# Performance work log

Hardware: AMD Instinct MI355X
Metric: run time of the kernel (lower is better)

The kernel has to match this reference:

```python
import jax, jax.numpy as jnp
import numpy as np

KS = 3          # ksize
PAD = 1         # (ksize-1)//2 * dilation, dilation=1

def setup_inputs() -> dict:
    key = jax.random.key(0)
    k1, k2, k3, k4 = jax.random.split(key, 4)
    B, NI, C, H, W = 4, 64, 64, 256, 256
    features = jax.random.normal(k1, (B, NI, H, W), jnp.float32)
    inpt = jax.random.normal(k2, (B, C, H, W), jnp.float32)
    # get_filter: Conv2d(ni, ksize**2, 3, padding=1 reflect, stride=1)
    w = jax.random.normal(k3, (KS * KS, NI, 3, 3), jnp.float32) * 0.05
    b = jax.random.normal(k4, (KS * KS,), jnp.float32) * 0.01
    return {"features": features, "inpt": inpt, "w": w, "b": b}

def reference(features, inpt, w, b):
    # 1) predict per-pixel filters: 3x3 conv with reflect padding
    fpad = jnp.pad(features, ((0, 0), (0, 0), (1, 1), (1, 1)), mode="reflect")
    ff = jax.lax.conv_general_dilated(
        fpad, w, window_strides=(1, 1), padding="VALID",
        dimension_numbers=("NCHW", "OIHW", "NCHW"),
    ) + b[None, :, None, None]                       # [B, 9, H, W]
    ff = jax.nn.softmax(ff, axis=1)                  # softmax over the 9 taps

    # 2) apply per-pixel filter to inpt (shared across channels)
    B, C, H, W = inpt.shape
    ipad = jnp.pad(inpt, ((0, 0), (0, 0), (PAD, PAD), (PAD, PAD)), mode="reflect")
    # unfold: taps in row-major (ki, kj) order, matching torch nn.Unfold
    patches = jnp.stack(
        [ipad[:, :, i:i + H, j:j + W] for i in range(KS) for j in range(KS)],
        axis=2,
    )                                                # [B, C, 9, H, W]
    # out[b,c,h,w] = sum_k patches[b,c,k,h,w] * ff[b,k,h,w]
    return jnp.einsum("bckhw,bkhw->bchw", patches, ff)
```

## Files before the change

### kernel.cpp

```cpp
#include <hip/hip_runtime.h>
#include <math.h>

#define BB 4
#define NI 64
#define CC 64
#define HH 256
#define WW 256

__device__ __forceinline__ int refl(int i, int n) {
    i = (i < 0) ? -i : i;
    return (i >= n) ? (2 * n - 2 - i) : i;
}

__global__ __launch_bounds__(256) void pff_fused(
    const float* __restrict__ features,
    const float* __restrict__ inpt,
    const float* __restrict__ wgt,
    const float* __restrict__ bias,
    float* __restrict__ out)
{
    const int tid = threadIdx.x;
    const int wx = blockIdx.x * 64 + (tid & 63);
    const int hy = blockIdx.y * 4 + (tid >> 6);
    const int b  = blockIdx.z;

    const int ih0 = refl(hy - 1, HH);
    const int ih1 = hy;
    const int ih2 = refl(hy + 1, HH);
    const int iw0 = refl(wx - 1, WW);
    const int iw1 = wx;
    const int iw2 = refl(wx + 1, WW);

    const int r0 = ih0 * WW, r1 = ih1 * WW, r2 = ih2 * WW;

    float acc[9];
    #pragma unroll
    for (int k = 0; k < 9; ++k) acc[k] = bias[k];

    const float* fb = features + (size_t)b * NI * HH * WW;
    for (int ni = 0; ni < NI; ++ni) {
        const float* fc = fb + (size_t)ni * HH * WW;
        float f[9];
        f[0] = fc[r0 + iw0]; f[1] = fc[r0 + iw1]; f[2] = fc[r0 + iw2];
        f[3] = fc[r1 + iw0]; f[4] = fc[r1 + iw1]; f[5] = fc[r1 + iw2];
        f[6] = fc[r2 + iw0]; f[7] = fc[r2 + iw1]; f[8] = fc[r2 + iw2];

        const float* wn = wgt + ni * 9;
        #pragma unroll
        for (int k = 0; k < 9; ++k) {
            const float* wk = wn + k * (NI * 9);
            #pragma unroll
            for (int t = 0; t < 9; ++t)
                acc[k] = fmaf(f[t], wk[t], acc[k]);
        }
    }

    float m = acc[0];
    #pragma unroll
    for (int k = 1; k < 9; ++k) m = fmaxf(m, acc[k]);
    float s = 0.f;
    #pragma unroll
    for (int k = 0; k < 9; ++k) { acc[k] = __expf(acc[k] - m); s += acc[k]; }
    const float inv = 1.f / s;
    #pragma unroll
    for (int k = 0; k < 9; ++k) acc[k] *= inv;

    const float* ib = inpt + (size_t)b * CC * HH * WW;
    float* ob = out + (size_t)b * CC * HH * WW;
    const size_t opix = (size_t)hy * WW + wx;
    for (int c = 0; c < CC; ++c) {
        const float* ic = ib + (size_t)c * HH * WW;
        float o = acc[0] * ic[r0 + iw0];
        o = fmaf(acc[1], ic[r0 + iw1], o);
        o = fmaf(acc[2], ic[r0 + iw2], o);
        o = fmaf(acc[3], ic[r1 + iw0], o);
        o = fmaf(acc[4], ic[r1 + iw1], o);
        o = fmaf(acc[5], ic[r1 + iw2], o);
        o = fmaf(acc[6], ic[r2 + iw0], o);
        o = fmaf(acc[7], ic[r2 + iw1], o);
        o = fmaf(acc[8], ic[r2 + iw2], o);
        ob[(size_t)c * HH * WW + opix] = o;
    }
}

extern "C" void kernel_launch(void* const* d_in, const int* in_sizes, int n_in,
                              void* d_out, int out_size, void* d_ws, size_t ws_size,
                              hipStream_t stream) {
    const float* features = (const float*)d_in[0];
    const float* inpt     = (const float*)d_in[1];
    const float* wgt      = (const float*)d_in[2];
    const float* bias     = (const float*)d_in[3];
    float* out            = (float*)d_out;

    dim3 grid(WW / 64, HH / 4, BB);
    dim3 block(256);
    pff_fused<<<grid, block, 0, stream>>>(features, inpt, wgt, bias, out);
}
```

Baseline: 83.08 us.

## Compute filter-prediction conv with bf16 MFMA from LDS-staged feature tiles

Replaces the scalar per-pixel 3x3x64 filter-prediction convolution with bf16 MFMA 16x16x32 instructions. Feature tiles with halo are staged into LDS as bf16, and the weights are pre-packed by a small prep kernel into an MFMA-ready table in workspace. Softmax is computed across lanes with shuffles, and the channel-application loop is split across waves with software prefetch of the next channel. This removes most of the FP32 FMA work and redundant global loads, at the cost of bf16 rounding in the logits and an extra kernel launch.

```diff
diff --git a/kernel.cpp b/kernel.cpp
--- a/kernel.cpp
+++ b/kernel.cpp
@@ -2,84 +2,170 @@
 #include <math.h>
 
 #define BB 4
-#define NI 64
+#define NIC 64
 #define CC 64
 #define HH 256
 #define WW 256
+#define HW (HH * WW)
+
+#define TCH 72
+
+typedef short sh8 __attribute__((ext_vector_type(8)));
+typedef float f32x4 __attribute__((ext_vector_type(4)));
 
 __device__ __forceinline__ int refl(int i, int n) {
     i = (i < 0) ? -i : i;
     return (i >= n) ? (2 * n - 2 - i) : i;
 }
+__device__ __forceinline__ unsigned short f2bf(float v) {
+    unsigned int x = __builtin_bit_cast(unsigned int, v);
+    return (unsigned short)((x + 0x7FFFu + ((x >> 16) & 1u)) >> 16);
+}
 
-__global__ __launch_bounds__(256) void pff_fused(
+__global__ void pff_prep(const float* __restrict__ wgt, uint4* __restrict__ wtab) {
+    int e = blockIdx.x * 256 + threadIdx.x;
+    if (e >= 18 * 64) return;
+    const int c = e >> 6, l = e & 63;
+    const int s = c >> 1, h = c & 1;
+    const int tap = l & 15, kg = l >> 4;
+    unsigned short bb16[8];
+    #pragma unroll
+    for (int j = 0; j < 8; ++j) {
+        const int ni = 32 * h + 8 * kg + j;
+        const float v = (tap <= 8) ? wgt[tap * 576 + ni * 9 + s] : 0.f;
+        bb16[j] = f2bf(v);
+    }
+    uint4 o;
+    o.x = bb16[0] | ((unsigned)bb16[1] << 16);
+    o.y = bb16[2] | ((unsigned)bb16[3] << 16);
+    o.z = bb16[4] | ((unsigned)bb16[5] << 16);
+    o.w = bb16[6] | ((unsigned)bb16[7] << 16);
+    wtab[e] = o;
+}
+
+__global__ __launch_bounds__(512) void pff_mfma(
     const float* __restrict__ features,
     const float* __restrict__ inpt,
-    const float* __restrict__ wgt,
     const float* __restrict__ bias,
+    const uint4* __restrict__ wtab,
     float* __restrict__ out)
 {
-    const int tid = threadIdx.x;
-    const int wx = blockIdx.x * 64 + (tid & 63);
-    const int hy = blockIdx.y * 4 + (tid >> 6);
-    const int b  = blockIdx.z;
+    __shared__ __align__(16) unsigned short T[4 * 66 * TCH];
+    __shared__ uint4 wtile[18 * 64];
+    __shared__ float ffl[9 * 128];
 
-    const int ih0 = refl(hy - 1, HH);
-    const int ih1 = hy;
-    const int ih2 = refl(hy + 1, HH);
-    const int iw0 = refl(wx - 1, WW);
-    const int iw1 = wx;
-    const int iw2 = refl(wx + 1, WW);
+    const int tid  = threadIdx.x;
+    const int wv   = __builtin_amdgcn_readfirstlane(tid >> 6);
+    const int lane = tid & 63;
+    const int W0 = blockIdx.x * 64;
+    const int H0 = blockIdx.y * 2;
+    const int bb = blockIdx.z;
 
-    const int r0 = ih0 * WW, r1 = ih1 * WW, r2 = ih2 * WW;
-
-    float acc[9];
+    const int kg  = lane >> 4;
+    const int pxl = lane & 15;
+    float bv4[4];
     #pragma unroll
-    for (int k = 0; k < 9; ++k) acc[k] = bias[k];
-
-    const float* fb = features + (size_t)b * NI * HH * WW;
-    for (int ni = 0; ni < NI; ++ni) {
-        const float* fc = fb + (size_t)ni * HH * WW;
-        float f[9];
-        f[0] = fc[r0 + iw0]; f[1] = fc[r0 + iw1]; f[2] = fc[r0 + iw2];
-        f[3] = fc[r1 + iw0]; f[4] = fc[r1 + iw1]; f[5] = fc[r1 + iw2];
-        f[6] = fc[r2 + iw0]; f[7] = fc[r2 + iw1]; f[8] = fc[r2 + iw2];
-
-        const float* wn = wgt + ni * 9;
-        #pragma unroll
-        for (int k = 0; k < 9; ++k) {
-            const float* wk = wn + k * (NI * 9);
-            #pragma unroll
-            for (int t = 0; t < 9; ++t)
-                acc[k] = fmaf(f[t], wk[t], acc[k]);
-        }
+    for (int j = 0; j < 4; ++j) {
+        const int tap = 4 * kg + j;
+        bv4[j] = bias[tap <= 8 ? tap : 8];
     }
 
-    float m = acc[0];
-    #pragma unroll
-    for (int k = 1; k < 9; ++k) m = fmaxf(m, acc[k]);
-    float s = 0.f;
-    #pragma unroll
-    for (int k = 0; k < 9; ++k) { acc[k] = __expf(acc[k] - m); s += acc[k]; }
-    const float inv = 1.f / s;
-    #pragma unroll
-    for (int k = 0; k < 9; ++k) acc[k] *= inv;
+    {
+        const int gc1 = refl(W0 - 1 + lane, WW);
+        const int gc2 = refl(W0 + 63 + lane, WW);
+        for (int it = wv; it < 256; it += 8) {
+            const int ch = it & 63, ri = it >> 6;
+            const int gr = refl(H0 - 1 + ri, HH);
+            const float* fp = features + ((bb * NIC + ch) * HH + gr) * WW;
+            const float v1 = fp[gc1];
+            T[(ri * 66 + lane) * TCH + ch] = f2bf(v1);
+            if (lane < 2) {
+                const float v2 = fp[gc2];
+                T[(ri * 66 + 64 + lane) * TCH + ch] = f2bf(v2);
+            }
+        }
+        for (int i = tid; i < 18 * 64; i += 512) wtile[i] = wtab[i];
+    }
+    __syncthreads();
 
-    const float* ib = inpt + (size_t)b * CC * HH * WW;
-    float* ob = out + (size_t)b * CC * HH * WW;
-    const size_t opix = (size_t)hy * WW + wx;
-    for (int c = 0; c < CC; ++c) {
-        const float* ic = ib + (size_t)c * HH * WW;
-        float o = acc[0] * ic[r0 + iw0];
-        o = fmaf(acc[1], ic[r0 + iw1], o);
-        o = fmaf(acc[2], ic[r0 + iw2], o);
-        o = fmaf(acc[3], ic[r1 + iw0], o);
-        o = fmaf(acc[4], ic[r1 + iw1], o);
-        o = fmaf(acc[5], ic[r1 + iw2], o);
-        o = fmaf(acc[6], ic[r2 + iw0], o);
-        o = fmaf(acc[7], ic[r2 + iw1], o);
-        o = fmaf(acc[8], ic[r2 + iw2], o);
-        ob[(size_t)c * HH * WW + opix] = o;
+    {
+        const int grow = wv & 1;
+        const int col0 = (wv >> 1) * 16;
+        f32x4 acc = {0.f, 0.f, 0.f, 0.f};
+        const int baseB = (grow * 66 + col0 + pxl) * TCH + 8 * kg;
+        #pragma unroll
+        for (int c = 0; c < 18; ++c) {
+            const int s = c >> 1, h = c & 1;
+            const int idx = baseB + ((s / 3) * 66 + (s % 3)) * TCH + 32 * h;
+            sh8 bv = *reinterpret_cast<const sh8*>(&T[idx]);
+            sh8 av = *reinterpret_cast<const sh8*>(&wtile[c * 64 + lane]);
+            acc = __builtin_amdgcn_mfma_f32_16x16x32_bf16(av, bv, acc, 0, 0, 0);
+        }
+        float lg[4];
+        bool val[4];
+        #pragma unroll
+        for (int j = 0; j < 4; ++j) {
+            const int tap = 4 * kg + j;
+            val[j] = (tap <= 8);
+            lg[j] = acc[j] + bv4[j];
+        }
+        float ml = -3e38f;
+        #pragma unroll
+        for (int j = 0; j < 4; ++j) ml = fmaxf(ml, val[j] ? lg[j] : -3e38f);
+        float m = fmaxf(ml, __shfl_xor(ml, 16));
+        m = fmaxf(m, __shfl_xor(m, 32));
+        float e[4], sl = 0.f;
+        #pragma unroll
+        for (int j = 0; j < 4; ++j) { e[j] = val[j] ? __expf(lg[j] - m) : 0.f; sl += e[j]; }
+        float s = sl + __shfl_xor(sl, 16);
+        s += __shfl_xor(s, 32);
+        const float inv = 1.f / s;
+        #pragma unroll
+        for (int j = 0; j < 4; ++j)
+            if (val[j]) ffl[(4 * kg + j) * 128 + grow * 64 + col0 + pxl] = e[j] * inv;
+    }
+    __syncthreads();
+
+    {
+        const int q = wv & 3;
+        const int r = wv >> 2;
+        const int wx = W0 + lane, py = H0 + r;
+        int go[9];
+        #pragma unroll
+        for (int i = 0; i < 3; ++i) {
+            const int rr = refl(py - 1 + i, HH) * WW;
+            #pragma unroll
+            for (int j = 0; j < 3; ++j) go[i * 3 + j] = rr + refl(wx - 1 + j, WW);
+        }
+        float ffv[9];
+        #pragma unroll
+        for (int k = 0; k < 9; ++k) ffv[k] = ffl[k * 128 + r * 64 + lane];
+
+        const float* ib = inpt + ((size_t)bb * CC + q * 16) * HW;
+        float* ob = out + ((size_t)bb * CC + q * 16) * HW + py * WW + wx;
+
+        float f[9], g[9];
+        #pragma unroll
+        for (int t = 0; t < 9; ++t) f[t] = ib[go[t]];
+        for (int chi = 0; chi < 16; ++chi) {
+            if (chi < 15) {
+                const float* i2 = ib + (size_t)(chi + 1) * HW;
+                #pragma unroll
+                for (int t = 0; t < 9; ++t) g[t] = i2[go[t]];
+            }
+            float o = ffv[0] * f[0];
+            o = fmaf(ffv[1], f[1], o);
+            o = fmaf(ffv[2], f[2], o);
+            o = fmaf(ffv[3], f[3], o);
+            o = fmaf(ffv[4], f[4], o);
+            o = fmaf(ffv[5], f[5], o);
+            o = fmaf(ffv[6], f[6], o);
+            o = fmaf(ffv[7], f[7], o);
+            o = fmaf(ffv[8], f[8], o);
+            ob[(size_t)chi * HW] = o;
+            #pragma unroll
+            for (int t = 0; t < 9; ++t) f[t] = g[t];
+        }
     }
 }
 
@@ -91,8 +177,11 @@
     const float* wgt      = (const float*)d_in[2];
     const float* bias     = (const float*)d_in[3];
     float* out            = (float*)d_out;
+    uint4* wtab           = (uint4*)d_ws;
 
-    dim3 grid(WW / 64, HH / 4, BB);
-    dim3 block(256);
-    pff_fused<<<grid, block, 0, stream>>>(features, inpt, wgt, bias, out);
+    pff_prep<<<dim3((18 * 64 + 255) / 256), dim3(256), 0, stream>>>(wgt, wtab);
+
+    dim3 grid(WW / 64, HH / 2, BB);
+    dim3 block(512);
+    pff_mfma<<<grid, block, 0, stream>>>(features, inpt, bias, wtab, out);
 }
```

After: 130.3 us. 1.57x slower.
